# Kernel tuning notes

Hardware: AMD Instinct MI355X
Metric: run time of the kernel (lower is better)

## Reference

```python
import jax, jax.numpy as jnp
import numpy as np

N, E, B, NUM_NODES = 80000, 1280000, 8, 10000
D_IN, H, EMB, ATT, OUT = 64, 64, 64, 64, 1


def setup_inputs() -> dict:
    key = jax.random.key(0)
    ks = jax.random.split(key, 12)
    x = jax.random.normal(ks[0], (N, D_IN), dtype=jnp.float32)
    edge_index = jax.random.randint(ks[1], (2, E), 0, N, dtype=jnp.int64)
    edge_weight = jax.random.uniform(ks[2], (E,), dtype=jnp.float32)
    batch = jnp.repeat(jnp.arange(B, dtype=jnp.int64), NUM_NODES)
    app_embedding = jax.random.normal(ks[3], (B, 1, EMB), dtype=jnp.float32)
    def lin(k, fi, fo):
        bound = 1.0 / np.sqrt(fi)
        k1, k2 = jax.random.split(k)
        W = jax.random.uniform(k1, (fi, fo), minval=-bound, maxval=bound, dtype=jnp.float32)
        b = jax.random.uniform(k2, (fo,), minval=-bound, maxval=bound, dtype=jnp.float32)
        return W, b
    W1, b1 = lin(ks[4], D_IN, H)
    W2, b2 = lin(ks[5], H, H)
    Wa, ba = lin(ks[6], H + EMB, ATT)
    Ws, bs = lin(ks[7], ATT, 1)
    Wo, bo = lin(ks[8], H, OUT)
    return dict(x=x, edge_index=edge_index, edge_weight=edge_weight, batch=batch,
                app_embedding=app_embedding, W1=W1, b1=b1, W2=W2, b2=b2,
                Wa=Wa, ba=ba, Ws=Ws, bs=bs, Wo=Wo, bo=bo)


def gcn_conv(x, row, col, ew, W, b):
    # PyG GCNConv: add self-loops (weight 1), symmetric normalization
    n = x.shape[0]
    xw = x @ W                                            # [N, H]
    deg = jax.ops.segment_sum(ew, col, num_segments=n) + 1.0  # self-loop adds 1
    dis = jax.lax.rsqrt(deg)                              # deg >= 1
    norm = dis[row] * ew * dis[col]                       # [E]
    agg = jax.ops.segment_sum(norm[:, None] * xw[row], col, num_segments=n)
    return agg + (dis * dis)[:, None] * xw + b            # self-loop term + bias


def reference(x, edge_index, edge_weight, batch, app_embedding,
              W1, b1, W2, b2, Wa, ba, Ws, bs, Wo, bo):
    row, col = edge_index[0], edge_index[1]
    h = jax.nn.relu(gcn_conv(x, row, col, edge_weight, W1, b1))
    h = jax.nn.relu(gcn_conv(h, row, col, edge_weight, W2, b2))
    emb = app_embedding[:, 0, :][batch]                   # [N, EMB]
    combined = jnp.concatenate([h, emb], axis=-1)         # [N, H+EMB]
    att_hidden = jax.nn.leaky_relu(combined @ Wa + ba, negative_slope=0.2)
    scores = att_hidden @ Ws + bs                         # [N, 1]
    weights = jax.nn.softmax(scores, axis=0)              # softmax over all nodes
    node_out = (weights * h) @ Wo + bo                    # [N, OUT=1]
    flat = node_out.reshape(-1)                           # [N] since OUT=1
    sums = jax.ops.segment_sum(flat, batch, num_segments=B)
    counts = jax.ops.segment_sum(jnp.ones_like(flat), batch, num_segments=B)
    return sums / counts                                  # global_mean_pool -> [B]
```

## Files before the change

kernel.cpp:

```cpp
#include <hip/hip_runtime.h>
#include <hip/hip_fp16.h>
#include <math.h>


#define DEG_SCALE 16777216.0f
#define DEG_INV   (1.0f / 16777216.0f)
#define M48       0xFFFFFFFFFFFFULL
#define MAXDEG    64

typedef struct __align__(8) { __half2 a, b; } half4_t;
typedef __attribute__((ext_vector_type(8))) _Float16 h8;
typedef __attribute__((ext_vector_type(4))) float f32x4;


__global__ __launch_bounds__(256) void front_kernel(
    const float* __restrict__ x, const float* __restrict__ W1,
    __half* __restrict__ Y, int N,
    const int* __restrict__ ei, const float* __restrict__ ew,
    unsigned long long* __restrict__ packed, unsigned int* __restrict__ epack2,
    int E, int nG) {
  int bid = (int)blockIdx.x;
  bool isGemm = (bid % 5 == 0) && (bid / 5 < nG);
  if (!isGemm) {
    int gBefore = (bid + 4) / 5; if (gBefore > nG) gBefore = nG;
    int di = bid - gBefore;
    int e = di * 256 + threadIdx.x;
    if (e >= E) return;
    int row = ei[e];
    int col = ei[E + e];
    float w = ew[e];
    unsigned long long q = (unsigned long long)(w * DEG_SCALE + 0.5f);
    unsigned long long old = atomicAdd(&packed[col], (1ULL << 48) | q);
    unsigned rank = (unsigned)(old >> 48);
    unsigned q15 = (unsigned)(w * 32768.0f + 0.5f);
    if (q15 > 32767u) q15 = 32767u;
    if (rank < MAXDEG)
      epack2[(size_t)col * MAXDEG + rank] = ((unsigned)row << 15) | q15;
    return;
  }
  int gb = bid / 5;
  __shared__ float wlds[64][65];
  int t = threadIdx.x;
  for (int i = t; i < 4096; i += 256) wlds[i >> 6][i & 63] = W1[i];
  __syncthreads();
  int lane = t & 63, wave = t >> 6;
  int sub = lane & 15, grp = lane >> 4;
  int r0 = gb * 64 + wave * 16;
  h8 bf[2][4];
#pragma unroll
  for (int kk = 0; kk < 2; ++kk)
#pragma unroll
    for (int f = 0; f < 4; ++f)
#pragma unroll
      for (int i = 0; i < 8; ++i)
        bf[kk][f][i] = (_Float16)wlds[kk * 32 + grp * 8 + i][f * 16 + sub];
  int arow = r0 + sub; if (arow >= N) arow = N - 1;
  const float4* xr = (const float4*)(x + (size_t)arow * 64 + grp * 8);
  float4 u0 = xr[0], u1 = xr[1];
  const float4* xr2 = (const float4*)(x + (size_t)arow * 64 + 32 + grp * 8);
  float4 v0 = xr2[0], v1 = xr2[1];
  h8 a0, a1;
  a0[0]=(_Float16)u0.x; a0[1]=(_Float16)u0.y; a0[2]=(_Float16)u0.z; a0[3]=(_Float16)u0.w;
  a0[4]=(_Float16)u1.x; a0[5]=(_Float16)u1.y; a0[6]=(_Float16)u1.z; a0[7]=(_Float16)u1.w;
  a1[0]=(_Float16)v0.x; a1[1]=(_Float16)v0.y; a1[2]=(_Float16)v0.z; a1[3]=(_Float16)v0.w;
  a1[4]=(_Float16)v1.x; a1[5]=(_Float16)v1.y; a1[6]=(_Float16)v1.z; a1[7]=(_Float16)v1.w;
  f32x4 zero = {0.f, 0.f, 0.f, 0.f};
  f32x4 acc[4] = {zero, zero, zero, zero};
#pragma unroll
  for (int f = 0; f < 4; ++f) {
    acc[f] = __builtin_amdgcn_mfma_f32_16x16x32_f16(a0, bf[0][f], acc[f], 0, 0, 0);
    acc[f] = __builtin_amdgcn_mfma_f32_16x16x32_f16(a1, bf[1][f], acc[f], 0, 0, 0);
  }
  _Float16* Yp = (_Float16*)Y;
#pragma unroll
  for (int f = 0; f < 4; ++f)
#pragma unroll
    for (int j = 0; j < 4; ++j) {
      int orow = r0 + grp * 4 + j;
      if (orow < N) Yp[(size_t)orow * 64 + f * 16 + sub] = (_Float16)acc[f][j];
    }
}

__global__ __launch_bounds__(256) void dis_scale_kernel(
    const unsigned long long* __restrict__ packed, __half* __restrict__ xw,
    float* __restrict__ dis, int N) {
  int idx4 = blockIdx.x * 256 + threadIdx.x;
  if (idx4 >= N * 16) return;
  int row = idx4 >> 4;
  int off = (idx4 & 15);
  unsigned long long p = packed[row];
  float d = rsqrtf((float)(long long)(p & M48) * DEG_INV + 1.0f);
  if (off == 0) dis[row] = d;
  half4_t* ptr = (half4_t*)(xw + (size_t)row * 64) + off;
  half4_t v = *ptr;
  float2 a = __half22float2(v.a), b = __half22float2(v.b);
  half4_t o;
  o.a = __floats2half2_rn(a.x * d, a.y * d);
  o.b = __floats2half2_rn(b.x * d, b.y * d);
  *ptr = o;
}

__global__ __launch_bounds__(256) void agg_fused_kernel(
    const __half* __restrict__ xw, const unsigned int* __restrict__ epack2,
    const unsigned long long* __restrict__ packed,
    const float* __restrict__ bias, __half* __restrict__ h, int N) {
  int wid = (blockIdx.x * 256 + threadIdx.x) >> 6;
  int lane = threadIdx.x & 63;
  if (wid >= N) return;
  int q = lane >> 4, sub = lane & 15;
  unsigned long long p = packed[wid];
  int cnt = (int)(p >> 48);
  if (cnt > MAXDEG) cnt = MAXDEG;
  float dis_c = rsqrtf((float)(long long)(p & M48) * DEG_INV + 1.0f);
  int start = wid * MAXDEG;
  int end = start + cnt;
  float ax = 0.f, ay = 0.f, az = 0.f, aw = 0.f;
  float bx = 0.f, by = 0.f, bz = 0.f, bw = 0.f;
  int t = start + q;
  for (; t + 12 < end; t += 16) {
    unsigned w0 = epack2[t];
    unsigned w1 = epack2[t + 4];
    unsigned w2 = epack2[t + 8];
    unsigned w3 = epack2[t + 12];
    const half4_t* p0 = (const half4_t*)(xw + ((size_t)(w0 >> 15)) * 64) + sub;
    const half4_t* p1 = (const half4_t*)(xw + ((size_t)(w1 >> 15)) * 64) + sub;
    const half4_t* p2 = (const half4_t*)(xw + ((size_t)(w2 >> 15)) * 64) + sub;
    const half4_t* p3 = (const half4_t*)(xw + ((size_t)(w3 >> 15)) * 64) + sub;
    half4_t v0 = *p0;
    half4_t v1 = *p1;
    half4_t v2 = *p2;
    half4_t v3 = *p3;
    float c0 = (float)(w0 & 0x7FFFu) * (1.0f / 32768.0f);
    float c1 = (float)(w1 & 0x7FFFu) * (1.0f / 32768.0f);
    float c2 = (float)(w2 & 0x7FFFu) * (1.0f / 32768.0f);
    float c3 = (float)(w3 & 0x7FFFu) * (1.0f / 32768.0f);
    float2 l0 = __half22float2(v0.a), m0 = __half22float2(v0.b);
    float2 l1 = __half22float2(v1.a), m1 = __half22float2(v1.b);
    float2 l2 = __half22float2(v2.a), m2 = __half22float2(v2.b);
    float2 l3 = __half22float2(v3.a), m3 = __half22float2(v3.b);
    ax = fmaf(c0, l0.x, ax); ay = fmaf(c0, l0.y, ay);
    az = fmaf(c0, m0.x, az); aw = fmaf(c0, m0.y, aw);
    bx = fmaf(c1, l1.x, bx); by = fmaf(c1, l1.y, by);
    bz = fmaf(c1, m1.x, bz); bw = fmaf(c1, m1.y, bw);
    ax = fmaf(c2, l2.x, ax); ay = fmaf(c2, l2.y, ay);
    az = fmaf(c2, m2.x, az); aw = fmaf(c2, m2.y, aw);
    bx = fmaf(c3, l3.x, bx); by = fmaf(c3, l3.y, by);
    bz = fmaf(c3, m3.x, bz); bw = fmaf(c3, m3.y, bw);
  }
  for (; t < end; t += 4) {
    unsigned w0 = epack2[t];
    const half4_t* p0 = (const half4_t*)(xw + ((size_t)(w0 >> 15)) * 64) + sub;
    half4_t v0 = *p0;
    float c0 = (float)(w0 & 0x7FFFu) * (1.0f / 32768.0f);
    float2 l0 = __half22float2(v0.a), m0 = __half22float2(v0.b);
    ax = fmaf(c0, l0.x, ax); ay = fmaf(c0, l0.y, ay);
    az = fmaf(c0, m0.x, az); aw = fmaf(c0, m0.y, aw);
  }
  ax += bx; ay += by; az += bz; aw += bw;
  ax += __shfl_xor(ax, 16, 64); ay += __shfl_xor(ay, 16, 64);
  az += __shfl_xor(az, 16, 64); aw += __shfl_xor(aw, 16, 64);
  ax += __shfl_xor(ax, 32, 64); ay += __shfl_xor(ay, 32, 64);
  az += __shfl_xor(az, 32, 64); aw += __shfl_xor(aw, 32, 64);
  if (q == 0) {
    half4_t self = *((const half4_t*)(xw + (size_t)wid * 64) + sub);
    float2 s0 = __half22float2(self.a), s1 = __half22float2(self.b);
    float4 bv = *((const float4*)bias + sub);
    float vx = fmaxf(dis_c * (ax + s0.x) + bv.x, 0.f);
    float vy = fmaxf(dis_c * (ay + s0.y) + bv.y, 0.f);
    float vz = fmaxf(dis_c * (az + s1.x) + bv.z, 0.f);
    float vw = fmaxf(dis_c * (aw + s1.y) + bv.w, 0.f);
    half4_t o;
    o.a = __floats2half2_rn(vx, vy);
    o.b = __floats2half2_rn(vz, vw);
    *((half4_t*)(h + (size_t)wid * 64) + sub) = o;
  }
}

__global__ __launch_bounds__(256) void gemm_mfma_f16_scaled(
    const __half* __restrict__ X, const float* __restrict__ W,
    const float* __restrict__ dis, __half* __restrict__ Y, int N) {
  __shared__ float wlds[64][65];
  int t = threadIdx.x;
  for (int i = t; i < 4096; i += 256) wlds[i >> 6][i & 63] = W[i];
  __syncthreads();
  int lane = t & 63, wave = t >> 6;
  int sub = lane & 15, grp = lane >> 4;
  int r0 = (int)blockIdx.x * 64 + wave * 16;
  h8 bf[2][4];
#pragma unroll
  for (int kk = 0; kk < 2; ++kk)
#pragma unroll
    for (int f = 0; f < 4; ++f)
#pragma unroll
      for (int i = 0; i < 8; ++i)
        bf[kk][f][i] = (_Float16)wlds[kk * 32 + grp * 8 + i][f * 16 + sub];
  int arow = r0 + sub; if (arow >= N) arow = N - 1;
  const _Float16* Xp = (const _Float16*)X;
  h8 a0 = *(const h8*)(Xp + (size_t)arow * 64 + grp * 8);
  h8 a1 = *(const h8*)(Xp + (size_t)arow * 64 + 32 + grp * 8);
  f32x4 zero = {0.f, 0.f, 0.f, 0.f};
  f32x4 acc[4] = {zero, zero, zero, zero};
#pragma unroll
  for (int f = 0; f < 4; ++f) {
    acc[f] = __builtin_amdgcn_mfma_f32_16x16x32_f16(a0, bf[0][f], acc[f], 0, 0, 0);
    acc[f] = __builtin_amdgcn_mfma_f32_16x16x32_f16(a1, bf[1][f], acc[f], 0, 0, 0);
  }
  _Float16* Yp = (_Float16*)Y;
#pragma unroll
  for (int j = 0; j < 4; ++j) {
    int orow = r0 + grp * 4 + j;
    if (orow < N) {
      float d = dis[orow];
#pragma unroll
      for (int f = 0; f < 4; ++f)
        Yp[(size_t)orow * 64 + f * 16 + sub] = (_Float16)(acc[f][j] * d);
    }
  }
}

__global__ __launch_bounds__(256) void pre_kernel(
    const float* __restrict__ emb, const float* __restrict__ Wa,
    const float* __restrict__ ba, float* __restrict__ pre, int B) {
  int t = blockIdx.x * 256 + threadIdx.x;
  if (t >= B * 64) return;
  int b = t >> 6, j = t & 63;
  float s = ba[j];
  for (int k = 0; k < 64; ++k)
    s = fmaf(emb[b * 64 + k], Wa[(64 + k) * 64 + j], s);
  pre[t] = s;
}

__global__ __launch_bounds__(256) void att_mfma_kernel(
    const __half* __restrict__ h2, const int* __restrict__ bat,
    const float* __restrict__ Wa, const float* __restrict__ Ws,
    const float* __restrict__ bs, const float* __restrict__ pre,
    const float* __restrict__ Wo,
    float* __restrict__ scores, float* __restrict__ dots,
    float* __restrict__ bmax, float* __restrict__ bsum, int N) {
  __shared__ float wlds[64][65];
  __shared__ float pr[8][64];
  __shared__ float wov[64];
  __shared__ float redm[4], reds[4];
  int t = threadIdx.x;
  for (int i = t; i < 4096; i += 256) wlds[i >> 6][i & 63] = Wa[i];
  for (int i = t; i < 512; i += 256) pr[i >> 6][i & 63] = pre[i];
  if (t < 64) wov[t] = Wo[t];
  __syncthreads();
  int lane = t & 63, wave = t >> 6;
  int sub = lane & 15, grp = lane >> 4;
  int r0 = (int)blockIdx.x * 64 + wave * 16;
  h8 bf[2][4];
#pragma unroll
  for (int kk = 0; kk < 2; ++kk)
#pragma unroll
    for (int f = 0; f < 4; ++f)
#pragma unroll
      for (int i = 0; i < 8; ++i)
        bf[kk][f][i] = (_Float16)wlds[kk * 32 + grp * 8 + i][f * 16 + sub];
  float wsf[4];
#pragma unroll
  for (int f = 0; f < 4; ++f) wsf[f] = Ws[f * 16 + sub];
  float bs0 = bs[0];
  int arow = r0 + sub; if (arow >= N) arow = N - 1;
  const _Float16* Xp = (const _Float16*)h2;
  h8 a0 = *(const h8*)(Xp + (size_t)arow * 64 + grp * 8);
  h8 a1 = *(const h8*)(Xp + (size_t)arow * 64 + 32 + grp * 8);
  float dp = 0.f;
#pragma unroll
  for (int i = 0; i < 8; ++i) {
    dp = fmaf((float)a0[i], wov[grp * 8 + i], dp);
    dp = fmaf((float)a1[i], wov[32 + grp * 8 + i], dp);
  }
  dp += __shfl_xor(dp, 16, 64);
  dp += __shfl_xor(dp, 32, 64);
  if (grp == 0 && r0 + sub < N) dots[r0 + sub] = dp;
  f32x4 zero = {0.f, 0.f, 0.f, 0.f};
  f32x4 acc[4] = {zero, zero, zero, zero};
#pragma unroll
  for (int f = 0; f < 4; ++f) {
    acc[f] = __builtin_amdgcn_mfma_f32_16x16x32_f16(a0, bf[0][f], acc[f], 0, 0, 0);
    acc[f] = __builtin_amdgcn_mfma_f32_16x16x32_f16(a1, bf[1][f], acc[f], 0, 0, 0);
  }
  float sloc[4];
  float mloc = -3.4e38f;
#pragma unroll
  for (int j = 0; j < 4; ++j) {
    int row = r0 + grp * 4 + j;
    int rc = (row < N) ? row : N - 1;
    int b = bat[rc];
    float s = 0.f;
#pragma unroll
    for (int f = 0; f < 4; ++f) {
      float v = acc[f][j] + pr[b][f * 16 + sub];
      v = (v > 0.f) ? v : 0.2f * v;
      s = fmaf(v, wsf[f], s);
    }
    s += __shfl_xor(s, 1, 64); s += __shfl_xor(s, 2, 64);
    s += __shfl_xor(s, 4, 64); s += __shfl_xor(s, 8, 64);
    s += bs0;
    if (sub == 0 && row < N) scores[row] = s;
    sloc[j] = (row < N) ? s : -3.4e38f;
    mloc = fmaxf(mloc, sloc[j]);
  }
  for (int off = 32; off; off >>= 1) mloc = fmaxf(mloc, __shfl_xor(mloc, off, 64));
  if (lane == 0) redm[wave] = mloc;
  __syncthreads();
  float bm = fmaxf(fmaxf(redm[0], redm[1]), fmaxf(redm[2], redm[3]));
  float e = 0.f;
  if (sub == 0) {
#pragma unroll
    for (int j = 0; j < 4; ++j)
      if (sloc[j] > -3.0e38f) e += expf(sloc[j] - bm);
  }
  for (int off = 32; off; off >>= 1) e += __shfl_xor(e, off, 64);
  if (lane == 0) reds[wave] = e;
  __syncthreads();
  if (t == 0) {
    bmax[blockIdx.x] = bm;
    bsum[blockIdx.x] = reds[0] + reds[1] + reds[2] + reds[3];
  }
}

__global__ __launch_bounds__(256) void softmax_final_kernel(
    const float* __restrict__ bmax, const float* __restrict__ bsum,
    int nb, float* __restrict__ red) {
  __shared__ float lds[4];
  __shared__ float Msh;
  int t = threadIdx.x;
  float m = -3.4e38f;
  for (int i = t; i < nb; i += 256) m = fmaxf(m, bmax[i]);
  for (int off = 32; off; off >>= 1) m = fmaxf(m, __shfl_down(m, off, 64));
  if ((t & 63) == 0) lds[t >> 6] = m;
  __syncthreads();
  if (t == 0) Msh = fmaxf(fmaxf(lds[0], lds[1]), fmaxf(lds[2], lds[3]));
  __syncthreads();
  float M = Msh;
  float a = 0.f;
  for (int i = t; i < nb; i += 256) a += bsum[i] * expf(bmax[i] - M);
  for (int off = 32; off; off >>= 1) a += __shfl_down(a, off, 64);
  if ((t & 63) == 0) lds[t >> 6] = a;
  __syncthreads();
  if (t == 0) { red[0] = M; red[1] = lds[0] + lds[1] + lds[2] + lds[3]; }
}

__global__ __launch_bounds__(256) void finalize_kernel(
    const float* __restrict__ scores, const float* __restrict__ dots,
    const int* __restrict__ batch, const float* __restrict__ red,
    float* __restrict__ acc, int N) {
  __shared__ int sb0;
  __shared__ float lds0[4], lds1[4];
  int t = threadIdx.x;
  int i0 = blockIdx.x * 256;
  if (t == 0) sb0 = batch[i0];
  __syncthreads();
  int i = i0 + t;
  float v0 = 0.f, v1 = 0.f;
  if (i < N) {
    float m = red[0];
    float inv = 1.0f / red[1];
    float val = expf(scores[i] - m) * inv * dots[i];
    int b = batch[i];
    if (b == sb0) v0 = val; else v1 = val;
  }
  for (int off = 32; off; off >>= 1) {
    v0 += __shfl_down(v0, off, 64);
    v1 += __shfl_down(v1, off, 64);
  }
  if ((t & 63) == 0) { lds0[t >> 6] = v0; lds1[t >> 6] = v1; }
  __syncthreads();
  if (t == 0) {
    float s0 = lds0[0] + lds0[1] + lds0[2] + lds0[3];
    float s1 = lds1[0] + lds1[1] + lds1[2] + lds1[3];
    atomicAdd(&acc[sb0], s0);
    if (sb0 + 1 < 8) atomicAdd(&acc[sb0 + 1], s1);
  }
}

__global__ __launch_bounds__(64) void out_kernel(
    const float* __restrict__ acc, const float* __restrict__ bo,
    float* __restrict__ out, int B, int nodes_per_batch) {
  int b = threadIdx.x;
  if (b >= B) return;
  out[b] = acc[b] / (float)nodes_per_batch + bo[0];
}

extern "C" void kernel_launch(void* const* d_in, const int* in_sizes, int n_in,
                              void* d_out, int out_size, void* d_ws, size_t ws_size,
                              hipStream_t stream) {
  const float* x   = (const float*)d_in[0];
  const int*   ei  = (const int*)d_in[1];
  const float* ew  = (const float*)d_in[2];
  const int*   bat = (const int*)d_in[3];
  const float* emb = (const float*)d_in[4];
  const float* W1  = (const float*)d_in[5];
  const float* b1  = (const float*)d_in[6];
  const float* W2  = (const float*)d_in[7];
  const float* b2  = (const float*)d_in[8];
  const float* Wa  = (const float*)d_in[9];
  const float* ba  = (const float*)d_in[10];
  const float* Ws  = (const float*)d_in[11];
  const float* bs  = (const float*)d_in[12];
  const float* Wo  = (const float*)d_in[13];
  const float* bo  = (const float*)d_in[14];
  float* out = (float*)d_out;

  const int N = in_sizes[0] / 64;
  const int E = in_sizes[2];
  const int B = in_sizes[4] / 64;

  float* ws = (float*)d_ws;
  size_t o = 0;
  unsigned long long* packed = (unsigned long long*)(ws + o); o += 2 * (size_t)N;
  float* accb = ws + o; o += 16;
  unsigned int* epack2 = (unsigned int*)(ws + o); o += (size_t)N * MAXDEG;
  __half* bufA   = (__half*)(ws + o); o += (size_t)N * 32;
  __half* bufB   = (__half*)(ws + o); o += (size_t)N * 32;
  float* dis     = ws + o; o += N;
  float* scores  = ws + o; o += N;
  float* dots    = ws + o; o += N;
  float* pre     = ws + o; o += 512;
  float* bmaxa   = ws + o; o += 2048;
  float* bsuma   = ws + o; o += 2048;
  float* red     = ws + o; o += 8;

  hipMemsetAsync(packed, 0, (size_t)(2 * N + 16) * sizeof(float), stream);

  int gE = (E + 255) / 256;
  int gN = (N + 255) / 256;
  int gW = (N * 64 + 255) / 256;
  int gM = (N + 63) / 64;
  int gS = (N * 16 + 255) / 256;

  front_kernel<<<gM + gE, 256, 0, stream>>>(x, W1, bufA, N, ei, ew, packed, epack2, E, gM);

  dis_scale_kernel<<<gS, 256, 0, stream>>>(packed, bufA, dis, N);

  agg_fused_kernel<<<gW, 256, 0, stream>>>(bufA, epack2, packed, b1, bufB, N);
  gemm_mfma_f16_scaled<<<gM, 256, 0, stream>>>(bufB, W2, dis, bufA, N);
  agg_fused_kernel<<<gW, 256, 0, stream>>>(bufA, epack2, packed, b2, bufB, N);

  pre_kernel<<<(B * 64 + 255) / 256, 256, 0, stream>>>(emb, Wa, ba, pre, B);
  att_mfma_kernel<<<gM, 256, 0, stream>>>(bufB, bat, Wa, Ws, bs, pre, Wo,
                                          scores, dots, bmaxa, bsuma, N);
  softmax_final_kernel<<<1, 256, 0, stream>>>(bmaxa, bsuma, gM, red);

  finalize_kernel<<<gN, 256, 0, stream>>>(scores, dots, bat, red, accb, N);
  out_kernel<<<1, 64, 0, stream>>>(accb, bo, out, B, N / B);
}
```

Baseline: 231.8 us.

## Fuse softmax-weighted pooling into attention kernel and widen gather loads to 16 bytes

The attention kernel now computes per-block exp-weighted partial sums for the two possible batch segments in each block. A single tail kernel rescales these by the global max and normalizer and writes the output, which removes the scores/dots round trip and the separate finalize and out kernels. The pre_kernel is merged into the dis-scale launch. The aggregation and scaling kernels switch from 8-byte half4 to 16-byte h8 loads, using 8 lanes per row instead of 16. Edge parallelism per row becomes 8 instead of 4 with less unrolling, and the tail assumes a block never spans more than two batch segments.

```diff
diff --git a/kernel.cpp b/kernel.cpp
--- a/kernel.cpp
+++ b/kernel.cpp
@@ -8,7 +8,6 @@
 #define M48       0xFFFFFFFFFFFFULL
 #define MAXDEG    64
 
-typedef struct __align__(8) { __half2 a, b; } half4_t;
 typedef __attribute__((ext_vector_type(8))) _Float16 h8;
 typedef __attribute__((ext_vector_type(4))) float f32x4;
 
@@ -81,22 +80,33 @@
     }
 }
 
-__global__ __launch_bounds__(256) void dis_scale_kernel(
+__global__ __launch_bounds__(256) void mid_kernel(
     const unsigned long long* __restrict__ packed, __half* __restrict__ xw,
-    float* __restrict__ dis, int N) {
-  int idx4 = blockIdx.x * 256 + threadIdx.x;
-  if (idx4 >= N * 16) return;
-  int row = idx4 >> 4;
-  int off = (idx4 & 15);
+    float* __restrict__ dis, int N,
+    const float* __restrict__ emb, const float* __restrict__ Wa,
+    const float* __restrict__ ba, float* __restrict__ pre, int B, int gS) {
+  if ((int)blockIdx.x >= gS) {
+    int t = ((int)blockIdx.x - gS) * 256 + threadIdx.x;
+    if (t >= B * 64) return;
+    int b = t >> 6, j = t & 63;
+    float s = ba[j];
+    for (int k = 0; k < 64; ++k)
+      s = fmaf(emb[b * 64 + k], Wa[(64 + k) * 64 + j], s);
+    pre[t] = s;
+    return;
+  }
+  int idx = blockIdx.x * 256 + threadIdx.x;
+  if (idx >= N * 8) return;
+  int row = idx >> 3;
+  int off = idx & 7;
   unsigned long long p = packed[row];
   float d = rsqrtf((float)(long long)(p & M48) * DEG_INV + 1.0f);
   if (off == 0) dis[row] = d;
-  half4_t* ptr = (half4_t*)(xw + (size_t)row * 64) + off;
-  half4_t v = *ptr;
-  float2 a = __half22float2(v.a), b = __half22float2(v.b);
-  half4_t o;
-  o.a = __floats2half2_rn(a.x * d, a.y * d);
-  o.b = __floats2half2_rn(b.x * d, b.y * d);
+  h8* ptr = (h8*)(xw + (size_t)row * 64) + off;
+  h8 v = *ptr;
+  h8 o;
+#pragma unroll
+  for (int i = 0; i < 8; ++i) o[i] = (_Float16)((float)v[i] * d);
   *ptr = o;
 }
 
@@ -107,72 +117,49 @@
   int wid = (blockIdx.x * 256 + threadIdx.x) >> 6;
   int lane = threadIdx.x & 63;
   if (wid >= N) return;
-  int q = lane >> 4, sub = lane & 15;
+  int q = lane >> 3, sub = lane & 7;
   unsigned long long p = packed[wid];
   int cnt = (int)(p >> 48);
   if (cnt > MAXDEG) cnt = MAXDEG;
   float dis_c = rsqrtf((float)(long long)(p & M48) * DEG_INV + 1.0f);
   int start = wid * MAXDEG;
   int end = start + cnt;
-  float ax = 0.f, ay = 0.f, az = 0.f, aw = 0.f;
-  float bx = 0.f, by = 0.f, bz = 0.f, bw = 0.f;
+  float acc[8];
+#pragma unroll
+  for (int i = 0; i < 8; ++i) acc[i] = 0.f;
   int t = start + q;
-  for (; t + 12 < end; t += 16) {
+  for (; t + 8 < end; t += 16) {
     unsigned w0 = epack2[t];
-    unsigned w1 = epack2[t + 4];
-    unsigned w2 = epack2[t + 8];
-    unsigned w3 = epack2[t + 12];
-    const half4_t* p0 = (const half4_t*)(xw + ((size_t)(w0 >> 15)) * 64) + sub;
-    const half4_t* p1 = (const half4_t*)(xw + ((size_t)(w1 >> 15)) * 64) + sub;
-    const half4_t* p2 = (const half4_t*)(xw + ((size_t)(w2 >> 15)) * 64) + sub;
-    const half4_t* p3 = (const half4_t*)(xw + ((size_t)(w3 >> 15)) * 64) + sub;
-    half4_t v0 = *p0;
-    half4_t v1 = *p1;
-    half4_t v2 = *p2;
-    half4_t v3 = *p3;
+    unsigned w1 = epack2[t + 8];
+    h8 v0 = *(const h8*)(xw + ((size_t)(w0 >> 15)) * 64 + sub * 8);
+    h8 v1 = *(const h8*)(xw + ((size_t)(w1 >> 15)) * 64 + sub * 8);
     float c0 = (float)(w0 & 0x7FFFu) * (1.0f / 32768.0f);
     float c1 = (float)(w1 & 0x7FFFu) * (1.0f / 32768.0f);
-    float c2 = (float)(w2 & 0x7FFFu) * (1.0f / 32768.0f);
-    float c3 = (float)(w3 & 0x7FFFu) * (1.0f / 32768.0f);
-    float2 l0 = __half22float2(v0.a), m0 = __half22float2(v0.b);
-    float2 l1 = __half22float2(v1.a), m1 = __half22float2(v1.b);
-    float2 l2 = __half22float2(v2.a), m2 = __half22float2(v2.b);
-    float2 l3 = __half22float2(v3.a), m3 = __half22float2(v3.b);
-    ax = fmaf(c0, l0.x, ax); ay = fmaf(c0, l0.y, ay);
-    az = fmaf(c0, m0.x, az); aw = fmaf(c0, m0.y, aw);
-    bx = fmaf(c1, l1.x, bx); by = fmaf(c1, l1.y, by);
-    bz = fmaf(c1, m1.x, bz); bw = fmaf(c1, m1.y, bw);
-    ax = fmaf(c2, l2.x, ax); ay = fmaf(c2, l2.y, ay);
-    az = fmaf(c2, m2.x, az); aw = fmaf(c2, m2.y, aw);
-    bx = fmaf(c3, l3.x, bx); by = fmaf(c3, l3.y, by);
-    bz = fmaf(c3, m3.x, bz); bw = fmaf(c3, m3.y, bw);
-  }
-  for (; t < end; t += 4) {
+#pragma unroll
+    for (int i = 0; i < 8; ++i) acc[i] = fmaf(c0, (float)v0[i], acc[i]);
+#pragma unroll
+    for (int i = 0; i < 8; ++i) acc[i] = fmaf(c1, (float)v1[i], acc[i]);
+  }
+  if (t < end) {
     unsigned w0 = epack2[t];
-    const half4_t* p0 = (const half4_t*)(xw + ((size_t)(w0 >> 15)) * 64) + sub;
-    half4_t v0 = *p0;
+    h8 v0 = *(const h8*)(xw + ((size_t)(w0 >> 15)) * 64 + sub * 8);
     float c0 = (float)(w0 & 0x7FFFu) * (1.0f / 32768.0f);
-    float2 l0 = __half22float2(v0.a), m0 = __half22float2(v0.b);
-    ax = fmaf(c0, l0.x, ax); ay = fmaf(c0, l0.y, ay);
-    az = fmaf(c0, m0.x, az); aw = fmaf(c0, m0.y, aw);
-  }
-  ax += bx; ay += by; az += bz; aw += bw;
-  ax += __shfl_xor(ax, 16, 64); ay += __shfl_xor(ay, 16, 64);
-  az += __shfl_xor(az, 16, 64); aw += __shfl_xor(aw, 16, 64);
-  ax += __shfl_xor(ax, 32, 64); ay += __shfl_xor(ay, 32, 64);
-  az += __shfl_xor(az, 32, 64); aw += __shfl_xor(aw, 32, 64);
+#pragma unroll
+    for (int i = 0; i < 8; ++i) acc[i] = fmaf(c0, (float)v0[i], acc[i]);
+  }
+#pragma unroll
+  for (int i = 0; i < 8; ++i) {
+    acc[i] += __shfl_xor(acc[i], 8, 64);
+    acc[i] += __shfl_xor(acc[i], 16, 64);
+    acc[i] += __shfl_xor(acc[i], 32, 64);
+  }
   if (q == 0) {
-    half4_t self = *((const half4_t*)(xw + (size_t)wid * 64) + sub);
-    float2 s0 = __half22float2(self.a), s1 = __half22float2(self.b);
-    float4 bv = *((const float4*)bias + sub);
-    float vx = fmaxf(dis_c * (ax + s0.x) + bv.x, 0.f);
-    float vy = fmaxf(dis_c * (ay + s0.y) + bv.y, 0.f);
-    float vz = fmaxf(dis_c * (az + s1.x) + bv.z, 0.f);
-    float vw = fmaxf(dis_c * (aw + s1.y) + bv.w, 0.f);
-    half4_t o;
-    o.a = __floats2half2_rn(vx, vy);
-    o.b = __floats2half2_rn(vz, vw);
-    *((half4_t*)(h + (size_t)wid * 64) + sub) = o;
+    h8 self = *(const h8*)(xw + (size_t)wid * 64 + sub * 8);
+    h8 o;
+#pragma unroll
+    for (int i = 0; i < 8; ++i)
+      o[i] = (_Float16)fmaxf(dis_c * (acc[i] + (float)self[i]) + bias[sub * 8 + i], 0.f);
+    *(h8*)(h + (size_t)wid * 64 + sub * 8) = o;
   }
 }
 
@@ -218,33 +205,23 @@
   }
 }
 
-__global__ __launch_bounds__(256) void pre_kernel(
-    const float* __restrict__ emb, const float* __restrict__ Wa,
-    const float* __restrict__ ba, float* __restrict__ pre, int B) {
-  int t = blockIdx.x * 256 + threadIdx.x;
-  if (t >= B * 64) return;
-  int b = t >> 6, j = t & 63;
-  float s = ba[j];
-  for (int k = 0; k < 64; ++k)
-    s = fmaf(emb[b * 64 + k], Wa[(64 + k) * 64 + j], s);
-  pre[t] = s;
-}
-
 __global__ __launch_bounds__(256) void att_mfma_kernel(
     const __half* __restrict__ h2, const int* __restrict__ bat,
     const float* __restrict__ Wa, const float* __restrict__ Ws,
     const float* __restrict__ bs, const float* __restrict__ pre,
     const float* __restrict__ Wo,
-    float* __restrict__ scores, float* __restrict__ dots,
-    float* __restrict__ bmax, float* __restrict__ bsum, int N) {
+    float* __restrict__ bmax, float* __restrict__ bsum,
+    float* __restrict__ pd0, float* __restrict__ pd1, int N) {
   __shared__ float wlds[64][65];
   __shared__ float pr[8][64];
   __shared__ float wov[64];
-  __shared__ float redm[4], reds[4];
+  __shared__ float redm[4], reds[4], redp0[4], redp1[4];
+  __shared__ int sb0sh;
   int t = threadIdx.x;
   for (int i = t; i < 4096; i += 256) wlds[i >> 6][i & 63] = Wa[i];
   for (int i = t; i < 512; i += 256) pr[i >> 6][i & 63] = pre[i];
   if (t < 64) wov[t] = Wo[t];
+  if (t == 0) sb0sh = bat[blockIdx.x * 64];
   __syncthreads();
   int lane = t & 63, wave = t >> 6;
   int sub = lane & 15, grp = lane >> 4;
@@ -273,7 +250,6 @@
   }
   dp += __shfl_xor(dp, 16, 64);
   dp += __shfl_xor(dp, 32, 64);
-  if (grp == 0 && r0 + sub < N) dots[r0 + sub] = dp;
   f32x4 zero = {0.f, 0.f, 0.f, 0.f};
   f32x4 acc[4] = {zero, zero, zero, zero};
 #pragma unroll
@@ -281,13 +257,16 @@
     acc[f] = __builtin_amdgcn_mfma_f32_16x16x32_f16(a0, bf[0][f], acc[f], 0, 0, 0);
     acc[f] = __builtin_amdgcn_mfma_f32_16x16x32_f16(a1, bf[1][f], acc[f], 0, 0, 0);
   }
+  int sb0 = sb0sh;
   float sloc[4];
+  int bl[4];
   float mloc = -3.4e38f;
 #pragma unroll
   for (int j = 0; j < 4; ++j) {
     int row = r0 + grp * 4 + j;
     int rc = (row < N) ? row : N - 1;
     int b = bat[rc];
+    bl[j] = b;
     float s = 0.f;
 #pragma unroll
     for (int f = 0; f < 4; ++f) {
@@ -298,7 +277,6 @@
     s += __shfl_xor(s, 1, 64); s += __shfl_xor(s, 2, 64);
     s += __shfl_xor(s, 4, 64); s += __shfl_xor(s, 8, 64);
     s += bs0;
-    if (sub == 0 && row < N) scores[row] = s;
     sloc[j] = (row < N) ? s : -3.4e38f;
     mloc = fmaxf(mloc, sloc[j]);
   }
@@ -306,82 +284,69 @@
   if (lane == 0) redm[wave] = mloc;
   __syncthreads();
   float bm = fmaxf(fmaxf(redm[0], redm[1]), fmaxf(redm[2], redm[3]));
-  float e = 0.f;
+  float dj[4];
+#pragma unroll
+  for (int j = 0; j < 4; ++j) dj[j] = __shfl(dp, grp * 4 + j, 64);
+  float es = 0.f, p0 = 0.f, p1 = 0.f;
   if (sub == 0) {
 #pragma unroll
-    for (int j = 0; j < 4; ++j)
-      if (sloc[j] > -3.0e38f) e += expf(sloc[j] - bm);
-  }
-  for (int off = 32; off; off >>= 1) e += __shfl_xor(e, off, 64);
-  if (lane == 0) reds[wave] = e;
+    for (int j = 0; j < 4; ++j) {
+      if (sloc[j] > -3.0e38f) {
+        float e = expf(sloc[j] - bm);
+        es += e;
+        float v = e * dj[j];
+        if (bl[j] == sb0) p0 += v; else p1 += v;
+      }
+    }
+  }
+  for (int off = 32; off; off >>= 1) {
+    es += __shfl_xor(es, off, 64);
+    p0 += __shfl_xor(p0, off, 64);
+    p1 += __shfl_xor(p1, off, 64);
+  }
+  if (lane == 0) { reds[wave] = es; redp0[wave] = p0; redp1[wave] = p1; }
   __syncthreads();
   if (t == 0) {
     bmax[blockIdx.x] = bm;
     bsum[blockIdx.x] = reds[0] + reds[1] + reds[2] + reds[3];
-  }
-}
-
-__global__ __launch_bounds__(256) void softmax_final_kernel(
+    pd0[blockIdx.x] = redp0[0] + redp0[1] + redp0[2] + redp0[3];
+    pd1[blockIdx.x] = redp1[0] + redp1[1] + redp1[2] + redp1[3];
+  }
+}
+
+__global__ __launch_bounds__(256) void tail_kernel(
     const float* __restrict__ bmax, const float* __restrict__ bsum,
-    int nb, float* __restrict__ red) {
+    const float* __restrict__ pd0, const float* __restrict__ pd1,
+    int nb, int npb, const float* __restrict__ bo, float* __restrict__ out, int B) {
   __shared__ float lds[4];
-  __shared__ float Msh;
+  __shared__ float Msh, Zsh;
+  __shared__ float accs[9];
   int t = threadIdx.x;
+  if (t < 9) accs[t] = 0.f;
   float m = -3.4e38f;
-  for (int i = t; i < nb; i += 256) m = fmaxf(m, bmax[i]);
-  for (int off = 32; off; off >>= 1) m = fmaxf(m, __shfl_down(m, off, 64));
+  for (int k = t; k < nb; k += 256) m = fmaxf(m, bmax[k]);
+  for (int off = 32; off; off >>= 1) m = fmaxf(m, __shfl_xor(m, off, 64));
   if ((t & 63) == 0) lds[t >> 6] = m;
   __syncthreads();
   if (t == 0) Msh = fmaxf(fmaxf(lds[0], lds[1]), fmaxf(lds[2], lds[3]));
   __syncthreads();
   float M = Msh;
-  float a = 0.f;
-  for (int i = t; i < nb; i += 256) a += bsum[i] * expf(bmax[i] - M);
-  for (int off = 32; off; off >>= 1) a += __shfl_down(a, off, 64);
-  if ((t & 63) == 0) lds[t >> 6] = a;
-  __syncthreads();
-  if (t == 0) { red[0] = M; red[1] = lds[0] + lds[1] + lds[2] + lds[3]; }
-}
-
-__global__ __launch_bounds__(256) void finalize_kernel(
-    const float* __restrict__ scores, const float* __restrict__ dots,
-    const int* __restrict__ batch, const float* __restrict__ red,
-    float* __restrict__ acc, int N) {
-  __shared__ int sb0;
-  __shared__ float lds0[4], lds1[4];
-  int t = threadIdx.x;
-  int i0 = blockIdx.x * 256;
-  if (t == 0) sb0 = batch[i0];
-  __syncthreads();
-  int i = i0 + t;
-  float v0 = 0.f, v1 = 0.f;
-  if (i < N) {
-    float m = red[0];
-    float inv = 1.0f / red[1];
-    float val = expf(scores[i] - m) * inv * dots[i];
-    int b = batch[i];
-    if (b == sb0) v0 = val; else v1 = val;
-  }
-  for (int off = 32; off; off >>= 1) {
-    v0 += __shfl_down(v0, off, 64);
-    v1 += __shfl_down(v1, off, 64);
-  }
-  if ((t & 63) == 0) { lds0[t >> 6] = v0; lds1[t >> 6] = v1; }
-  __syncthreads();
-  if (t == 0) {
-    float s0 = lds0[0] + lds0[1] + lds0[2] + lds0[3];
-    float s1 = lds1[0] + lds1[1] + lds1[2] + lds1[3];
-    atomicAdd(&acc[sb0], s0);
-    if (sb0 + 1 < 8) atomicAdd(&acc[sb0 + 1], s1);
-  }
-}
-
-__global__ __launch_bounds__(64) void out_kernel(
-    const float* __restrict__ acc, const float* __restrict__ bo,
-    float* __restrict__ out, int B, int nodes_per_batch) {
-  int b = threadIdx.x;
-  if (b >= B) return;
-  out[b] = acc[b] / (float)nodes_per_batch + bo[0];
+  float z = 0.f;
+  for (int k = t; k < nb; k += 256) {
+    float e = expf(bmax[k] - M);
+    z += bsum[k] * e;
+    int b0 = (k * 64) / npb;
+    float v0 = pd0[k] * e;
+    float v1 = pd1[k] * e;
+    if (v0 != 0.f) atomicAdd(&accs[b0], v0);
+    if (v1 != 0.f) atomicAdd(&accs[b0 + 1], v1);
+  }
+  for (int off = 32; off; off >>= 1) z += __shfl_xor(z, off, 64);
+  if ((t & 63) == 0) lds[t >> 6] = z;
+  __syncthreads();
+  if (t == 0) Zsh = lds[0] + lds[1] + lds[2] + lds[3];
+  __syncthreads();
+  if (t < B) out[t] = accs[t] / Zsh / (float)npb + bo[0];
 }
 
 extern "C" void kernel_launch(void* const* d_in, const int* in_sizes, int n_in,
@@ -411,39 +376,33 @@
   float* ws = (float*)d_ws;
   size_t o = 0;
   unsigned long long* packed = (unsigned long long*)(ws + o); o += 2 * (size_t)N;
-  float* accb = ws + o; o += 16;
   unsigned int* epack2 = (unsigned int*)(ws + o); o += (size_t)N * MAXDEG;
   __half* bufA   = (__half*)(ws + o); o += (size_t)N * 32;
   __half* bufB   = (__half*)(ws + o); o += (size_t)N * 32;
   float* dis     = ws + o; o += N;
-  float* scores  = ws + o; o += N;
-  float* dots    = ws + o; o += N;
   float* pre     = ws + o; o += 512;
   float* bmaxa   = ws + o; o += 2048;
   float* bsuma   = ws + o; o += 2048;
-  float* red     = ws + o; o += 8;
-
-  hipMemsetAsync(packed, 0, (size_t)(2 * N + 16) * sizeof(float), stream);
+  float* pd0a    = ws + o; o += 2048;
+  float* pd1a    = ws + o; o += 2048;
+
+  hipMemsetAsync(packed, 0, (size_t)(2 * N) * sizeof(float), stream);
 
   int gE = (E + 255) / 256;
-  int gN = (N + 255) / 256;
   int gW = (N * 64 + 255) / 256;
   int gM = (N + 63) / 64;
-  int gS = (N * 16 + 255) / 256;
+  int gS = (N * 8 + 255) / 256;
+  int gP = (B * 64 + 255) / 256;
 
   front_kernel<<<gM + gE, 256, 0, stream>>>(x, W1, bufA, N, ei, ew, packed, epack2, E, gM);
 
-  dis_scale_kernel<<<gS, 256, 0, stream>>>(packed, bufA, dis, N);
+  mid_kernel<<<gS + gP, 256, 0, stream>>>(packed, bufA, dis, N, emb, Wa, ba, pre, B, gS);
 
   agg_fused_kernel<<<gW, 256, 0, stream>>>(bufA, epack2, packed, b1, bufB, N);
   gemm_mfma_f16_scaled<<<gM, 256, 0, stream>>>(bufB, W2, dis, bufA, N);
   agg_fused_kernel<<<gW, 256, 0, stream>>>(bufA, epack2, packed, b2, bufB, N);
 
-  pre_kernel<<<(B * 64 + 255) / 256, 256, 0, stream>>>(emb, Wa, ba, pre, B);
   att_mfma_kernel<<<gM, 256, 0, stream>>>(bufB, bat, Wa, Ws, bs, pre, Wo,
-                                          scores, dots, bmaxa, bsuma, N);
-  softmax_final_kernel<<<1, 256, 0, stream>>>(bmaxa, bsuma, gM, red);
-
-  finalize_kernel<<<gN, 256, 0, stream>>>(scores, dots, bat, red, accb, N);
-  out_kernel<<<1, 64, 0, stream>>>(accb, bo, out, B, N / B);
-}
+                                          bmaxa, bsuma, pd0a, pd1a, N);
+  tail_kernel<<<1, 256, 0, stream>>>(bmaxa, bsuma, pd0a, pd1a, gM, N / B, bo, out, B);
+}
```

Result: faster. 199.4 us (median of 2 runs) (-14.0%).
